# Optimization experiments

Measured on AMD Instinct MI355X. Metric: run time of the kernel, lower is better.

The kernel has to match this reference:

```python
import jax, jax.numpy as jnp
import numpy as np

B, T, W, HP = 1, 64, 88, 48   # batch, frames, pitches, hidden_per_pitch
NU, NH, K = 24, 4, 25          # n_unit, n_heads, neighborhood window
HD = NU // NH                  # head dim = 6
HL = NU // 2                   # LSTM hidden per direction = 12


def _lstm_bidir(x, w_ih, w_hh, b_ih, b_hh):
    # x: [N, T, In]; w_ih: [2, 4*HL, In]; w_hh: [2, 4*HL, HL]; biases: [2, 4*HL]
    N = x.shape[0]
    def run(Wih, Whh, bih, bhh, reverse):
        def step(carry, xt):
            h, c = carry
            g = xt @ Wih.T + h @ Whh.T + bih + bhh
            i, f, gg, o = jnp.split(g, 4, axis=-1)  # torch gate order i,f,g,o
            c = jax.nn.sigmoid(f) * c + jax.nn.sigmoid(i) * jnp.tanh(gg)
            h = jax.nn.sigmoid(o) * jnp.tanh(c)
            return (h, c), h
        init = (jnp.zeros((N, HL), x.dtype), jnp.zeros((N, HL), x.dtype))
        _, ys = jax.lax.scan(step, init, jnp.swapaxes(x, 0, 1), reverse=reverse)
        return jnp.swapaxes(ys, 0, 1)
    return jnp.concatenate([run(w_ih[0], w_hh[0], b_ih[0], b_hh[0], False),
                            run(w_ih[1], w_hh[1], b_ih[1], b_hh[1], True)], axis=-1)


def _natten2d(x, qkv_w, qkv_b, rpb, proj_w, proj_b):
    # Neighborhood attention over 2D grid [B, Hh, Ww] with KxK window clamped at borders.
    Bn, Hh, Ww, C = x.shape
    qkv = (x @ qkv_w.T + qkv_b).reshape(Bn, Hh, Ww, 3, NH, HD)
    q = qkv[..., 0, :, :] * (HD ** -0.5)
    k = qkv[..., 1, :, :]
    v = qkv[..., 2, :, :]
    half = K // 2
    ar = jnp.arange(K)
    idx_i = jnp.clip(jnp.arange(Hh) - half, 0, Hh - K)[:, None] + ar  # [Hh,K]
    idx_j = jnp.clip(jnp.arange(Ww) - half, 0, Ww - K)[:, None] + ar  # [Ww,K]
    kg = k[:, idx_i][:, :, :, idx_j]  # [B,Hh,K,Ww,K,NH,HD]
    vg = v[:, idx_i][:, :, :, idx_j]
    ri = idx_i - jnp.arange(Hh)[:, None] + (K - 1)  # relative pos bias indices [Hh,K]
    rj = idx_j - jnp.arange(Ww)[:, None] + (K - 1)  # [Ww,K]
    bias = rpb[:, ri][:, :, :, rj]                  # [NH,Hh,K,Ww,K]
    logits = jnp.einsum('bijnd,biajcnd->bnijac', q, kg)
    logits = logits + jnp.transpose(bias, (0, 1, 3, 2, 4))[None]
    attn = jax.nn.softmax(logits.reshape(Bn, NH, Hh, Ww, K * K), axis=-1)
    attn = attn.reshape(Bn, NH, Hh, Ww, K, K)
    out = jnp.einsum('bnijac,biajcnd->bijnd', attn, vg).reshape(Bn, Hh, Ww, C)
    return out @ proj_w.T + proj_b


def _forward(features, condition, mask, emb, w_ih_l0, w_hh_l0, b_ih_l0, b_hh_l0,
             w_ih_l1, w_hh_l1, b_ih_l1, b_hh_l1, qkv_w, qkv_b, rpb, proj_w, proj_b,
             out_w, out_b):
    # concat: [B,T,88,HP] + [B,T,88,4] + [B,T,88,1] -> [B,T,88,HP+5]
    cat = jnp.concatenate([jnp.transpose(features, (0, 1, 3, 2)), emb[condition],
                           mask[..., None]], axis=-1)
    x = jnp.transpose(cat, (0, 2, 1, 3)).reshape(B * W, T, HP + 5)  # pitchwise LSTM
    x = _lstm_bidir(x, w_ih_l0, w_hh_l0, b_ih_l0, b_hh_l0)
    x = _lstm_bidir(x, w_ih_l1, w_hh_l1, b_ih_l1, b_hh_l1)
    x = jnp.transpose(x.reshape(B, W, T, NU), (0, 2, 1, 3))  # [B,T,88,NU]
    for _ in range(2):  # n_layers=2; Sequential(*[m]*2) => SHARED weights
        x = _natten2d(x, qkv_w, qkv_b, rpb, proj_w, proj_b)
    return x @ out_w.T + out_b  # [B,T,88,5]


def setup_inputs():
    ks = jax.random.split(jax.random.key(0), 24)
    def unif(k, shape, fan):
        s = 1.0 / np.sqrt(fan)
        return jax.random.uniform(k, shape, jnp.float32, -s, s)
    return {
        'features': jax.random.normal(ks[0], (B, T, HP, W), jnp.float32),
        'condition': jax.random.randint(ks[1], (B, T, W), 0, 5),
        'mask': jax.random.uniform(ks[2], (B, T, W), jnp.float32),
        'emb': jax.random.normal(ks[3], (5, 4), jnp.float32),
        'w_ih_l0': unif(ks[4], (2, 4 * HL, HP + 5), HL),
        'w_hh_l0': unif(ks[5], (2, 4 * HL, HL), HL),
        'b_ih_l0': unif(ks[6], (2, 4 * HL), HL),
        'b_hh_l0': unif(ks[7], (2, 4 * HL), HL),
        'w_ih_l1': unif(ks[8], (2, 4 * HL, 2 * HL), HL),
        'w_hh_l1': unif(ks[9], (2, 4 * HL, HL), HL),
        'b_ih_l1': unif(ks[10], (2, 4 * HL), HL),
        'b_hh_l1': unif(ks[11], (2, 4 * HL), HL),
        'qkv_w': unif(ks[12], (3 * NU, NU), NU),
        'qkv_b': unif(ks[13], (3 * NU,), NU),
        'rpb': jax.random.normal(ks[14], (NH, 2 * K - 1, 2 * K - 1), jnp.float32) * 0.02,
        'proj_w': unif(ks[15], (NU, NU), NU),
        'proj_b': unif(ks[16], (NU,), NU),
        'out_w': unif(ks[17], (5, NU), NU),
        'out_b': unif(ks[18], (5,), NU),
    }


def reference(features, condition, mask, emb, w_ih_l0, w_hh_l0, b_ih_l0, b_hh_l0,
              w_ih_l1, w_hh_l1, b_ih_l1, b_hh_l1, qkv_w, qkv_b, rpb, proj_w, proj_b,
              out_w, out_b):
    return _forward(features, condition, mask, emb, w_ih_l0, w_hh_l0, b_ih_l0, b_hh_l0,
                    w_ih_l1, w_hh_l1, b_ih_l1, b_hh_l1, qkv_w, qkv_b, rpb,
                    proj_w, proj_b, out_w, out_b)
```

## Files before the change

kernel.cpp:

```cpp
#include <hip/hip_runtime.h>
#include <hip/hip_bf16.h>

#define NPIX (64*88)
#define NSEQ 88
#define TT 64
#define F0 53
#define GATES 48
#define LOG2E 1.4426950408889634f

typedef __hip_bfloat16 bf16;

__device__ __forceinline__ float frcp(float x){ return __builtin_amdgcn_rcpf(x); }
__device__ __forceinline__ float fexp2(float x){ return __builtin_amdgcn_exp2f(x); }
__device__ __forceinline__ float blo(unsigned u){ return __uint_as_float(u<<16); }
__device__ __forceinline__ float bhi(unsigned u){ return __uint_as_float(u & 0xffff0000u); }

__device__ __forceinline__ float rl(float v, int l){
  return __int_as_float(__builtin_amdgcn_readlane(__float_as_int(v), l));
}
template<int K> __device__ __forceinline__ float qbcast(float v){
  constexpr int ctrl = K | (K<<2) | (K<<4) | (K<<6);
  return __int_as_float(__builtin_amdgcn_update_dpp(0, __float_as_int(v), ctrl, 0xf, 0xf, true));
}

__device__ __forceinline__ void lstm_dir(const float* __restrict__ whh,
    const float* gb_base, float* ybuf, int d, int lane){
  int u = lane >> 2, grp = lane & 3;
  int uc = (u < 12) ? u : 11;
  int j = grp*12 + uc;
  float w[12];
  const float* wb = whh + (d*GATES + j)*12;
  #pragma unroll
  for (int m=0;m<12;++m) w[m] = wb[m]*LOG2E;
  float negs = (grp==2) ? -2.f : -1.f;
  float amul = (grp==2) ?  2.f :  1.f;
  float aadd = (grp==2) ? -1.f :  0.f;
  const float* gb = gb_base + (d*TT)*49 + j;
  float hval = 0.f, cval = 0.f;
  int t0 = d ? (TT-1) : 0;
  float gnext = gb[t0*49];
  bool wr = (grp==0) && (u < 12);
  for (int s=0;s<TT;++s){
    int t = d ? (TT-1-s) : s;
    float gg = gnext;
    int tn = d ? max(TT-2-s,0) : min(s+1,TT-1);
    gnext = gb[tn*49];
    float h0=rl(hval,0),  h1=rl(hval,4),  h2=rl(hval,8),   h3=rl(hval,12);
    float h4=rl(hval,16), h5=rl(hval,20), h6=rl(hval,24),  h7=rl(hval,28);
    float h8=rl(hval,32), h9=rl(hval,36), h10=rl(hval,40), h11=rl(hval,44);
    float a0 = gg + h0*w[0] + h4*w[4] + h8*w[8];
    float a1 = h1*w[1] + h5*w[5] + h9*w[9];
    float a2 = h2*w[2] + h6*w[6] + h10*w[10];
    float a3 = h3*w[3] + h7*w[7] + h11*w[11];
    float dot = (a0+a1)+(a2+a3);
    float act = amul*frcp(1.f + fexp2(negs*dot)) + aadd;
    float ai = qbcast<0>(act);
    float af = qbcast<1>(act);
    float ag = qbcast<2>(act);
    float ao = qbcast<3>(act);
    float cn = af*cval + ai*ag;
    float th = 2.f*frcp(1.f + fexp2(-2.885390081777927f*cn)) - 1.f;
    hval = ao*th; cval = cn;
    if (wr) ybuf[t*25 + d*12 + u] = hval;
  }
}

__global__ __launch_bounds__(1024, 4) void k_core(
    const float* __restrict__ feat, const int* __restrict__ cond,
    const float* __restrict__ mask, const float* __restrict__ emb,
    const float* __restrict__ wih0, const float* __restrict__ whh0,
    const float* __restrict__ bih0, const float* __restrict__ bhh0,
    const float* __restrict__ wih1, const float* __restrict__ whh1,
    const float* __restrict__ bih1, const float* __restrict__ bhh1,
    const float* __restrict__ qkv_w, const float* __restrict__ qkv_b,
    float* __restrict__ q, bf16* __restrict__ kh, bf16* __restrict__ vh){
  int n = (blockIdx.x & 7)*11 + (blockIdx.x >> 3);
  int tid = threadIdx.x;
  int wave = tid >> 6; int lane = tid & 63;
  __shared__ float smem[12864];
  float* gbuf = smem;
  float* sx   = smem + 6272;
  float* y0   = smem + 6272+3392;
  float* y1   = smem + 6272+4992;
  float* outb = smem;

  for (int idx = tid; idx < TT*F0; idx += 1024){
    int t = idx / F0, f = idx - t*F0;
    float v;
    if (f < 48)      v = feat[(t*48 + f)*88 + n];
    else if (f < 52) v = emb[cond[t*88+n]*4 + (f-48)];
    else             v = mask[t*88+n];
    sx[idx] = v;
  }
  __syncthreads();

  {
    int wu = __builtin_amdgcn_readfirstlane(wave);
    int dd = wu >> 3, jg = wu & 7;
    const float* w0 = wih0 + (dd*GATES + jg*6)*F0;
    const float* xr = sx + lane*F0;
    float a0[6], a1[6];
    #pragma unroll
    for (int k=0;k<6;++k){
      int j = dd*GATES + jg*6 + k;
      a0[k] = bih0[j] + bhh0[j];
      a1[k] = 0.f;
    }
    #pragma unroll
    for (int f=0; f<52; f+=2){
      float x0 = xr[f], x1 = xr[f+1];
      #pragma unroll
      for (int k=0;k<6;++k){
        a0[k] += x0*w0[k*F0+f];
        a1[k] += x1*w0[k*F0+f+1];
      }
    }
    {
      float x0 = xr[52];
      #pragma unroll
      for (int k=0;k<6;++k) a0[k] += x0*w0[k*F0+52];
    }
    float* go = gbuf + (dd*TT + lane)*49 + jg*6;
    #pragma unroll
    for (int k=0;k<6;++k) go[k] = (a0[k] + a1[k])*LOG2E;
  }
  __syncthreads();

  if (wave < 2) lstm_dir(whh0, gbuf, y0, wave, lane);
  __syncthreads();

  {
    int wu = __builtin_amdgcn_readfirstlane(wave);
    int dd = wu >> 3, jg = wu & 7;
    const float* w1p = wih1 + (dd*GATES + jg*6)*24;
    const float* xr = y0 + lane*25;
    float a0[6], a1[6];
    #pragma unroll
    for (int k=0;k<6;++k){
      int j = dd*GATES + jg*6 + k;
      a0[k] = bih1[j] + bhh1[j];
      a1[k] = 0.f;
    }
    #pragma unroll
    for (int c=0; c<24; c+=2){
      float x0 = xr[c], x1 = xr[c+1];
      #pragma unroll
      for (int k=0;k<6;++k){
        a0[k] += x0*w1p[k*24+c];
        a1[k] += x1*w1p[k*24+c+1];
      }
    }
    float* go = gbuf + (dd*TT + lane)*49 + jg*6;
    #pragma unroll
    for (int k=0;k<6;++k) go[k] = (a0[k] + a1[k])*LOG2E;
  }
  __syncthreads();

  if (wave < 2) lstm_dir(whh1, gbuf, y1, wave, lane);
  __syncthreads();

  if (wave < 12){
    int wu = __builtin_amdgcn_readfirstlane(wave);
    int g0 = wu*6;
    const float* qw = qkv_w + g0*24;
    const float* xr = y1 + lane*25;
    float a0[6], a1[6];
    #pragma unroll
    for (int k=0;k<6;++k){ a0[k] = qkv_b[g0+k]; a1[k] = 0.f; }
    #pragma unroll
    for (int c=0; c<24; c+=2){
      float x0 = xr[c], x1 = xr[c+1];
      #pragma unroll
      for (int k=0;k<6;++k){
        a0[k] += x0*qw[k*24+c];
        a1[k] += x1*qw[k*24+c+1];
      }
    }
    float* oo = outb + lane*73 + g0;
    #pragma unroll
    for (int k=0;k<6;++k) oo[k] = a0[k] + a1[k];
  }
  __syncthreads();

  for (int idx = tid; idx < TT*72; idx += 1024){
    int gq = idx % 72; int t = idx / 72;
    int p = t*88 + n;
    float acc = outb[t*73 + gq];
    int s = gq/24, rem = gq - s*24;
    if (s==0) q[p*24+rem] = acc*0.4082482904638631f;
    else {
      int hh = rem/6, pos = rem - hh*6;
      bf16* dst = (s==1) ? kh : vh;
      dst[((size_t)hh*NPIX + p)*8 + pos] = __float2bfloat16(acc);
    }
  }
}

__global__ __launch_bounds__(1024, 8) void k_nat(
    const float* __restrict__ q, const bf16* __restrict__ kh,
    const bf16* __restrict__ vh, const float* __restrict__ rpb,
    float* __restrict__ ao){
  int bid = blockIdx.x;
  int h = bid / 88; int t = bid - h*88;
  int ti = t / 11, tj = t - ti*11;
  int i0 = ti*8, j0 = tj*8;
  int tid = threadIdx.x;
  int w = tid >> 6; int lane = tid & 63;
  int osi = min(max(i0-12,0),39);
  int osj = min(max(j0-12,0),63);

  __shared__ unsigned lds[8609];
  unsigned* kt = lds;
  unsigned* vt = lds + 3104;
  float*    rb = (float*)(lds + 6208);
  float*  pbuf = (float*)lds;

  {
    int a = tid >> 5, b = tid & 31;
    int gi = min(osi + a, 63), gj = min(osj + b, 87);
    const uint4* kg = (const uint4*)kh;
    const uint4* vg = (const uint4*)vh;
    int src = h*NPIX + gi*88 + gj;
    uint4 kr = kg[src];
    uint4 vr = vg[src];
    int o = a*97 + b*3;
    kt[o] = kr.x; kt[o+1] = kr.y; kt[o+2] = kr.z;
    vt[o] = vr.x; vt[o+1] = vr.y; vt[o+2] = vr.z;
  }
  for (int idx = tid; idx < 2401; idx += 1024){
    rb[idx] = rpb[h*2401 + idx] * LOG2E;
  }
  __syncthreads();

  int pi = i0 + (lane >> 3), pj = j0 + (lane & 7);
  int p = pi*88 + pj;
  int si = min(max(pi-12,0),39), sj = min(max(pj-12,0),63);
  int kbase = (si - osi)*97 + (sj - osj)*3;
  int rbase = (si - pi + 24)*49 + (sj - pj + 24);

  float qv[6];
  const float* qp = q + p*24 + h*6;
  #pragma unroll
  for (int d=0; d<6; ++d) qv[d] = qp[d]*LOG2E;

  float m2 = -1e30f, s = 0.f;
  float acc[6] = {0,0,0,0,0,0};

  int a = 0, b = w;
  while (a < 25){
    int o = kbase + a*97 + b*3;
    unsigned k0 = kt[o], k1 = kt[o+1], k2 = kt[o+2];
    float bias = rb[rbase + a*49 + b];
    float lg = fmaf(qv[0], blo(k0), bias);
    lg = fmaf(qv[1], bhi(k0), lg);
    lg = fmaf(qv[2], blo(k1), lg);
    lg = fmaf(qv[3], bhi(k1), lg);
    lg = fmaf(qv[4], blo(k2), lg);
    lg = fmaf(qv[5], bhi(k2), lg);
    bool up = (lg - m2) > 8.f;
    if (__any(up)){
      float sc = up ? fexp2(m2 - lg) : 1.f;
      s *= sc;
      #pragma unroll
      for (int d=0; d<6; ++d) acc[d] *= sc;
      m2 = up ? lg : m2;
    }
    float pe = fexp2(lg - m2);
    s += pe;
    unsigned v0 = vt[o], v1 = vt[o+1], v2 = vt[o+2];
    acc[0] += pe*blo(v0); acc[1] += pe*bhi(v0);
    acc[2] += pe*blo(v1); acc[3] += pe*bhi(v1);
    acc[4] += pe*blo(v2); acc[5] += pe*bhi(v2);
    b += 16; if (b >= 25){ b -= 25; ++a; }
  }

  __syncthreads();
  if (w > 0){
    int pb = (w-1)*512 + lane;
    pbuf[pb]      = m2;
    pbuf[pb+64]   = s;
    #pragma unroll
    for (int d=0; d<6; ++d) pbuf[pb + (2+d)*64] = acc[d];
  }
  __syncthreads();
  if (w == 0){
    float M = m2, S = s;
    float A[6];
    #pragma unroll
    for (int d=0; d<6; ++d) A[d] = acc[d];
    #pragma unroll
    for (int k=0; k<15; ++k){
      int pb = k*512 + lane;
      float mk = pbuf[pb];
      float sk = pbuf[pb+64];
      float Mn = fmaxf(M, mk);
      float sc1 = fexp2(M - Mn);
      float sc2 = fexp2(mk - Mn);
      S = S*sc1 + sk*sc2;
      #pragma unroll
      for (int d=0; d<6; ++d)
        A[d] = A[d]*sc1 + pbuf[pb + (2+d)*64]*sc2;
      M = Mn;
    }
    float inv = frcp(S);
    float* aop = ao + p*24 + h*6;
    #pragma unroll
    for (int d=0; d<6; ++d) aop[d] = A[d]*inv;
  }
}

__global__ __launch_bounds__(1024) void k_ep0(const float* __restrict__ ao,
    const float* __restrict__ pw, const float* __restrict__ pb,
    const float* __restrict__ qkv_w, const float* __restrict__ qkv_b,
    float* __restrict__ q2, bf16* __restrict__ kh2, bf16* __restrict__ vh2){
  int p0 = blockIdx.x*64; int tid = threadIdx.x;
  __shared__ float ar[64*25];
  __shared__ float xr[64*25];
  for (int idx = tid; idx < 64*24; idx += 1024){
    int px = idx / 24, c = idx - px*24;
    ar[px*25 + c] = ao[p0*24 + idx];
  }
  __syncthreads();
  for (int idx = tid; idx < 64*24; idx += 1024){
    int px = idx / 24, c = idx - px*24;
    float acc = pb[c];
    const float* wr = pw + c*24;
    const float* arow = ar + px*25;
    #pragma unroll
    for (int k=0;k<24;++k) acc += arow[k]*wr[k];
    xr[px*25 + c] = acc;
  }
  __syncthreads();
  for (int idx = tid; idx < 64*72; idx += 1024){
    int px = idx / 72, g = idx - px*72;
    float acc = qkv_b[g];
    const float* wr = qkv_w + g*24;
    const float* xrow = xr + px*25;
    #pragma unroll
    for (int k=0;k<24;++k) acc += xrow[k]*wr[k];
    int p = p0 + px;
    int sg = g/24, rem = g - sg*24;
    if (sg==0) q2[p*24+rem] = acc*0.4082482904638631f;
    else {
      int hh = rem/6, pos = rem - hh*6;
      bf16* dst = (sg==1) ? kh2 : vh2;
      dst[((size_t)hh*NPIX + p)*8 + pos] = __float2bfloat16(acc);
    }
  }
}

__global__ __launch_bounds__(1024) void k_ep1(const float* __restrict__ ao,
    const float* __restrict__ pw, const float* __restrict__ pb,
    const float* __restrict__ ow, const float* __restrict__ ob,
    float* __restrict__ out){
  int p0 = blockIdx.x*64; int tid = threadIdx.x;
  __shared__ float ar[64*25];
  __shared__ float xr[64*25];
  for (int idx = tid; idx < 64*24; idx += 1024){
    int px = idx / 24, c = idx - px*24;
    ar[px*25 + c] = ao[p0*24 + idx];
  }
  __syncthreads();
  for (int idx = tid; idx < 64*24; idx += 1024){
    int px = idx / 24, c = idx - px*24;
    float acc = pb[c];
    const float* wr = pw + c*24;
    const float* arow = ar + px*25;
    #pragma unroll
    for (int k=0;k<24;++k) acc += arow[k]*wr[k];
    xr[px*25 + c] = acc;
  }
  __syncthreads();
  if (tid < 64*5){
    int px = tid / 5, c = tid - px*5;
    float acc = ob[c];
    const float* wr = ow + c*24;
    const float* xrow = xr + px*25;
    #pragma unroll
    for (int k=0;k<24;++k) acc += xrow[k]*wr[k];
    out[(p0 + px)*5 + c] = acc;
  }
}

extern "C" void kernel_launch(void* const* d_in, const int* in_sizes, int n_in,
                              void* d_out, int out_size, void* d_ws, size_t ws_size,
                              hipStream_t stream) {
  const float* feat    = (const float*)d_in[0];
  const int*   cond    = (const int*)  d_in[1];
  const float* mask    = (const float*)d_in[2];
  const float* emb     = (const float*)d_in[3];
  const float* w_ih_l0 = (const float*)d_in[4];
  const float* w_hh_l0 = (const float*)d_in[5];
  const float* b_ih_l0 = (const float*)d_in[6];
  const float* b_hh_l0 = (const float*)d_in[7];
  const float* w_ih_l1 = (const float*)d_in[8];
  const float* w_hh_l1 = (const float*)d_in[9];
  const float* b_ih_l1 = (const float*)d_in[10];
  const float* b_hh_l1 = (const float*)d_in[11];
  const float* qkv_w   = (const float*)d_in[12];
  const float* qkv_b   = (const float*)d_in[13];
  const float* rpb     = (const float*)d_in[14];
  const float* proj_w  = (const float*)d_in[15];
  const float* proj_b  = (const float*)d_in[16];
  const float* out_w   = (const float*)d_in[17];
  const float* out_b   = (const float*)d_in[18];
  float* out = (float*)d_out;

  float* ws  = (float*)d_ws;
  float* Q1  = ws;
  float* Q2  = Q1 + 135168;
  float* AO  = Q2 + 135168;
  bf16*  KH1 = (bf16*)(AO + 135168);
  bf16*  VH1 = KH1 + 180224;
  bf16*  KH2 = VH1 + 180224;
  bf16*  VH2 = KH2 + 180224;

  k_core<<<NSEQ, 1024, 0, stream>>>(
      feat, cond, mask, emb,
      w_ih_l0, w_hh_l0, b_ih_l0, b_hh_l0,
      w_ih_l1, w_hh_l1, b_ih_l1, b_hh_l1,
      qkv_w, qkv_b, Q1, KH1, VH1);

  k_nat<<<4*88, 1024, 0, stream>>>(Q1, KH1, VH1, rpb, AO);

  k_ep0<<<NPIX/64, 1024, 0, stream>>>(AO, proj_w, proj_b, qkv_w, qkv_b,
      Q2, KH2, VH2);

  k_nat<<<4*88, 1024, 0, stream>>>(Q2, KH2, VH2, rpb, AO);

  k_ep1<<<NPIX/64, 1024, 0, stream>>>(AO, proj_w, proj_b, out_w, out_b, out);
}
```

Baseline: 186.7 us.

## Map one wave per query pixel in neighborhood attention with wave reductions

Restructures the neighborhood-attention kernel so each 64-lane wave handles one query pixel. Lanes split the 625 neighbors, and a two-pass softmax runs with DPP wave max and sum reductions. This replaces the old scheme of one lane per pixel with online softmax and a cross-wave merge through LDS. Tiles shrink to 2x4 pixels in 512-thread blocks, giving 2816 blocks with an interleaved block order. K and V are now stored as uint4 in LDS, and the relative position bias is read directly from global memory. The grid is much larger and tile halos are loaded redundantly, and only lane 0 writes each output.

```diff
diff --git a/kernel.cpp b/kernel.cpp
--- a/kernel.cpp
+++ b/kernel.cpp
@@ -21,6 +21,24 @@
 template<int K> __device__ __forceinline__ float qbcast(float v){
   constexpr int ctrl = K | (K<<2) | (K<<4) | (K<<6);
   return __int_as_float(__builtin_amdgcn_update_dpp(0, __float_as_int(v), ctrl, 0xf, 0xf, true));
+}
+
+template<int CTRL> __device__ __forceinline__ float dpp_add(float v){
+  return v + __int_as_float(__builtin_amdgcn_update_dpp(0, __float_as_int(v), CTRL, 0xf, 0xf, true));
+}
+template<int CTRL> __device__ __forceinline__ float dpp_max(float v){
+  int vi = __float_as_int(v);
+  return fmaxf(v, __int_as_float(__builtin_amdgcn_update_dpp(vi, vi, CTRL, 0xf, 0xf, false)));
+}
+__device__ __forceinline__ float wred_sum(float v){
+  v = dpp_add<0x111>(v); v = dpp_add<0x112>(v); v = dpp_add<0x114>(v); v = dpp_add<0x118>(v);
+  v = dpp_add<0x142>(v); v = dpp_add<0x143>(v);
+  return rl(v,63);
+}
+__device__ __forceinline__ float wred_max(float v){
+  v = dpp_max<0x111>(v); v = dpp_max<0x112>(v); v = dpp_max<0x114>(v); v = dpp_max<0x118>(v);
+  v = dpp_max<0x142>(v); v = dpp_max<0x143>(v);
+  return rl(v,63);
 }
 
 __device__ __forceinline__ void lstm_dir(const float* __restrict__ whh,
@@ -196,116 +214,88 @@
   }
 }
 
-__global__ __launch_bounds__(1024, 8) void k_nat(
+__global__ __launch_bounds__(512, 8) void k_nat(
     const float* __restrict__ q, const bf16* __restrict__ kh,
     const bf16* __restrict__ vh, const float* __restrict__ rpb,
     float* __restrict__ ao){
   int bid = blockIdx.x;
-  int h = bid / 88; int t = bid - h*88;
-  int ti = t / 11, tj = t - ti*11;
-  int i0 = ti*8, j0 = tj*8;
+  int b = (bid & 7)*352 + (bid >> 3);
+  int h = b / 704; int t = b - h*704;
+  int ti = t / 22, tj = t - ti*22;
+  int i0 = ti*2, j0 = tj*4;
   int tid = threadIdx.x;
   int w = tid >> 6; int lane = tid & 63;
-  int osi = min(max(i0-12,0),39);
-  int osj = min(max(j0-12,0),63);
-
-  __shared__ unsigned lds[8609];
-  unsigned* kt = lds;
-  unsigned* vt = lds + 3104;
-  float*    rb = (float*)(lds + 6208);
-  float*  pbuf = (float*)lds;
-
-  {
-    int a = tid >> 5, b = tid & 31;
-    int gi = min(osi + a, 63), gj = min(osj + b, 87);
-    const uint4* kg = (const uint4*)kh;
-    const uint4* vg = (const uint4*)vh;
-    int src = h*NPIX + gi*88 + gj;
-    uint4 kr = kg[src];
-    uint4 vr = vg[src];
-    int o = a*97 + b*3;
-    kt[o] = kr.x; kt[o+1] = kr.y; kt[o+2] = kr.z;
-    vt[o] = vr.x; vt[o+1] = vr.y; vt[o+2] = vr.z;
-  }
-  for (int idx = tid; idx < 2401; idx += 1024){
-    rb[idx] = rpb[h*2401 + idx] * LOG2E;
-  }
-  __syncthreads();
-
-  int pi = i0 + (lane >> 3), pj = j0 + (lane & 7);
+  int osi = min(max(i0-12,0), 38);
+  int osj = min(max(j0-12,0), 60);
+
+  __shared__ uint4 kt[728];
+  __shared__ uint4 vt[728];
+
+  const uint4* kg = (const uint4*)kh;
+  const uint4* vg = (const uint4*)vh;
+  for (int idx = tid; idx < 728; idx += 512){
+    int a = idx / 28, cc = idx - a*28;
+    int src = h*NPIX + (osi + a)*88 + (osj + cc);
+    kt[idx] = kg[src];
+    vt[idx] = vg[src];
+  }
+  __syncthreads();
+
+  int pi = i0 + (w >> 2), pj = j0 + (w & 3);
   int p = pi*88 + pj;
   int si = min(max(pi-12,0),39), sj = min(max(pj-12,0),63);
-  int kbase = (si - osi)*97 + (sj - osj)*3;
-  int rbase = (si - pi + 24)*49 + (sj - pj + 24);
+  int kbase = (si - osi)*28 + (sj - osj);
+  int rbi = si - pi + 24, rbj = sj - pj + 24;
+  const float* rpbh = rpb + (h*49 + rbi)*49 + rbj;
 
   float qv[6];
-  const float* qp = q + p*24 + h*6;
-  #pragma unroll
-  for (int d=0; d<6; ++d) qv[d] = qp[d]*LOG2E;
-
-  float m2 = -1e30f, s = 0.f;
+  #pragma unroll
+  for (int d=0; d<6; ++d) qv[d] = q[p*24 + h*6 + d];
+
+  float lgv[10];
+  float lmax = -1e30f;
+  #pragma unroll
+  for (int it=0; it<10; ++it){
+    int nb = lane + it*64;
+    bool valid = nb < 625;
+    int nbc = valid ? nb : 624;
+    int a = nbc/25, cc = nbc - a*25;
+    uint4 kk = kt[kbase + a*28 + cc];
+    float lg = qv[0]*blo(kk.x)+qv[1]*bhi(kk.x)+qv[2]*blo(kk.y)
+             + qv[3]*bhi(kk.y)+qv[4]*blo(kk.z)+qv[5]*bhi(kk.z);
+    lg += rpbh[a*49 + cc];
+    lg = valid ? lg : -1e30f;
+    lgv[it] = lg;
+    lmax = fmaxf(lmax, lg);
+  }
+  lmax = wred_max(lmax);
+  float lsum = 0.f;
+  #pragma unroll
+  for (int it=0; it<10; ++it){
+    float pe = __expf(lgv[it]-lmax);
+    lgv[it] = pe; lsum += pe;
+  }
+  lsum = wred_sum(lsum);
   float acc[6] = {0,0,0,0,0,0};
-
-  int a = 0, b = w;
-  while (a < 25){
-    int o = kbase + a*97 + b*3;
-    unsigned k0 = kt[o], k1 = kt[o+1], k2 = kt[o+2];
-    float bias = rb[rbase + a*49 + b];
-    float lg = fmaf(qv[0], blo(k0), bias);
-    lg = fmaf(qv[1], bhi(k0), lg);
-    lg = fmaf(qv[2], blo(k1), lg);
-    lg = fmaf(qv[3], bhi(k1), lg);
-    lg = fmaf(qv[4], blo(k2), lg);
-    lg = fmaf(qv[5], bhi(k2), lg);
-    bool up = (lg - m2) > 8.f;
-    if (__any(up)){
-      float sc = up ? fexp2(m2 - lg) : 1.f;
-      s *= sc;
-      #pragma unroll
-      for (int d=0; d<6; ++d) acc[d] *= sc;
-      m2 = up ? lg : m2;
-    }
-    float pe = fexp2(lg - m2);
-    s += pe;
-    unsigned v0 = vt[o], v1 = vt[o+1], v2 = vt[o+2];
-    acc[0] += pe*blo(v0); acc[1] += pe*bhi(v0);
-    acc[2] += pe*blo(v1); acc[3] += pe*bhi(v1);
-    acc[4] += pe*blo(v2); acc[5] += pe*bhi(v2);
-    b += 16; if (b >= 25){ b -= 25; ++a; }
-  }
-
-  __syncthreads();
-  if (w > 0){
-    int pb = (w-1)*512 + lane;
-    pbuf[pb]      = m2;
-    pbuf[pb+64]   = s;
-    #pragma unroll
-    for (int d=0; d<6; ++d) pbuf[pb + (2+d)*64] = acc[d];
-  }
-  __syncthreads();
-  if (w == 0){
-    float M = m2, S = s;
-    float A[6];
-    #pragma unroll
-    for (int d=0; d<6; ++d) A[d] = acc[d];
-    #pragma unroll
-    for (int k=0; k<15; ++k){
-      int pb = k*512 + lane;
-      float mk = pbuf[pb];
-      float sk = pbuf[pb+64];
-      float Mn = fmaxf(M, mk);
-      float sc1 = fexp2(M - Mn);
-      float sc2 = fexp2(mk - Mn);
-      S = S*sc1 + sk*sc2;
-      #pragma unroll
-      for (int d=0; d<6; ++d)
-        A[d] = A[d]*sc1 + pbuf[pb + (2+d)*64]*sc2;
-      M = Mn;
-    }
-    float inv = frcp(S);
+  #pragma unroll
+  for (int it=0; it<10; ++it){
+    int nb = lane + it*64;
+    int nbc = (nb < 625) ? nb : 624;
+    int a = nbc/25, cc = nbc - a*25;
+    uint4 vv = vt[kbase + a*28 + cc];
+    float pe = lgv[it];
+    acc[0] += pe*blo(vv.x); acc[1] += pe*bhi(vv.x);
+    acc[2] += pe*blo(vv.y); acc[3] += pe*bhi(vv.y);
+    acc[4] += pe*blo(vv.z); acc[5] += pe*bhi(vv.z);
+  }
+  float inv = frcp(lsum);
+  #pragma unroll
+  for (int d=0; d<6; ++d) acc[d] = wred_sum(acc[d])*inv;
+
+  if (lane == 0){
     float* aop = ao + p*24 + h*6;
     #pragma unroll
-    for (int d=0; d<6; ++d) aop[d] = A[d]*inv;
+    for (int d=0; d<6; ++d) aop[d] = acc[d];
   }
 }
 
@@ -421,12 +411,12 @@
       w_ih_l1, w_hh_l1, b_ih_l1, b_hh_l1,
       qkv_w, qkv_b, Q1, KH1, VH1);
 
-  k_nat<<<4*88, 1024, 0, stream>>>(Q1, KH1, VH1, rpb, AO);
+  k_nat<<<8*352, 512, 0, stream>>>(Q1, KH1, VH1, rpb, AO);
 
   k_ep0<<<NPIX/64, 1024, 0, stream>>>(AO, proj_w, proj_b, qkv_w, qkv_b,
       Q2, KH2, VH2);
 
-  k_nat<<<4*88, 1024, 0, stream>>>(Q2, KH2, VH2, rpb, AO);
+  k_nat<<<8*352, 512, 0, stream>>>(Q2, KH2, VH2, rpb, AO);
 
   k_ep1<<<NPIX/64, 1024, 0, stream>>>(AO, proj_w, proj_b, out_w, out_b, out);
 }
```

Result: faster. 177.6 us (-4.9%).
